# Kernel tuning notes

Measured on AMD Instinct MI355X. Metric: run time of the kernel, lower is better.

The kernel has to match this reference:

```python
import jax, jax.numpy as jnp
import numpy as np

D = 128      # embedding_dim
H = 8        # n_heads
L = 2        # n_encode_layers
FF = 512     # feed-forward hidden (4*D, AM default)
CLIP = 10.0  # tanh_clipping
EPS = 1e-5


def setup_inputs() -> dict:
    key = jax.random.key(0)
    ks = jax.random.split(key, 24)
    B, N = 32, 1000
    Nt = N + 2  # 2 depots + customers

    def w(k, shape, fan_in):
        return (jax.random.normal(k, shape, jnp.float32) / np.float32(np.sqrt(fan_in)))

    inp = {}
    inp["depot"] = jax.random.uniform(ks[0], (B, 2, 2), jnp.float32)
    inp["loc"] = jax.random.uniform(ks[1], (B, N, 2), jnp.float32)
    inp["demand"] = jax.random.uniform(ks[2], (B, N), jnp.float32)
    inp["mask"] = jax.random.randint(ks[3], (B, Nt), 0, 2) == 1
    # init embeddings
    inp["W_init_node"] = w(ks[4], (3, D), 3)
    inp["b_init_node"] = jnp.zeros((D,), jnp.float32)
    inp["W_init_depot"] = w(ks[5], (2, D), 2)
    inp["b_init_depot"] = jnp.zeros((D,), jnp.float32)
    # encoder layers (stacked over L)
    inp["enc_Wqkv"] = w(ks[6], (L, D, 3 * D), D)
    inp["enc_Wo"] = w(ks[7], (L, D, D), D)
    inp["enc_W1"] = w(ks[8], (L, D, FF), D)
    inp["enc_b1"] = jnp.zeros((L, FF), jnp.float32)
    inp["enc_W2"] = w(ks[9], (L, FF, D), FF)
    inp["enc_b2"] = jnp.zeros((L, D), jnp.float32)
    inp["bn1_s"] = jnp.ones((L, D), jnp.float32)
    inp["bn1_b"] = jnp.zeros((L, D), jnp.float32)
    inp["bn2_s"] = jnp.ones((L, D), jnp.float32)
    inp["bn2_b"] = jnp.zeros((L, D), jnp.float32)
    # decoder precompute / pointer attention
    inp["W_proj_node"] = w(ks[10], (D, 3 * D), D)   # project_node_embeddings_p2v
    inp["W_fixed_ctx"] = w(ks[11], (D, D), D)       # project_node_query_context
    inp["W_step_ctx"] = w(ks[12], (D, D), D)        # project_step_context_p2v
    inp["W_out"] = w(ks[13], (D, D), D)             # project_out_p2v
    return inp


def _bn(x, s, b):
    # BatchNorm1d over flattened (batch*nodes), training-mode stats, affine
    m = x.mean((0, 1))
    v = x.var((0, 1))
    return s * (x - m) * jax.lax.rsqrt(v + EPS) + b


def _mha(x, Wqkv, Wo):
    B, N, _ = x.shape
    dk = D // H
    q, k, v = jnp.split(x @ Wqkv, 3, axis=-1)

    def heads(t):
        return t.reshape(B, N, H, dk).transpose(0, 2, 1, 3)  # [B,H,N,dk]

    q, k, v = heads(q), heads(k), heads(v)
    attn = jax.nn.softmax(jnp.einsum('bhqd,bhkd->bhqk', q, k) / np.float32(np.sqrt(dk)), axis=-1)
    o = jnp.einsum('bhqk,bhkd->bhqd', attn, v).transpose(0, 2, 1, 3).reshape(B, N, D)
    return o @ Wo


def reference(depot, loc, demand, mask,
              W_init_node, b_init_node, W_init_depot, b_init_depot,
              enc_Wqkv, enc_Wo, enc_W1, enc_b1, enc_W2, enc_b2,
              bn1_s, bn1_b, bn2_s, bn2_b,
              W_proj_node, W_fixed_ctx, W_step_ctx, W_out):
    B = loc.shape[0]
    NEG = jnp.float32(-1e9)
    # --- init embeddings: depots via Linear(2,D), nodes via Linear(3,D) on (x,y,demand)
    depot_emb = depot @ W_init_depot + b_init_depot                      # [B,2,D]
    node_feat = jnp.concatenate([loc, demand[..., None]], -1)            # [B,N,3]
    node_emb = node_feat @ W_init_node + b_init_node                     # [B,N,D]
    h = jnp.concatenate([depot_emb, node_emb], 1)                        # [B,Nt,D]
    # --- graph encoder: L x (MHA + BN skip, FF + BN skip)
    for l in range(L):
        h = _bn(h + _mha(h, enc_Wqkv[l], enc_Wo[l]), bn1_s[l], bn1_b[l])
        ff = jax.nn.relu(h @ enc_W1[l] + enc_b1[l]) @ enc_W2[l] + enc_b2[l]
        h = _bn(h + ff, bn2_s[l], bn2_b[l])
    # --- fixed precompute (AttentionModelFixed)
    graph_embed = h.mean(1)                                              # [B,D]
    fixed_ctx = graph_embed @ W_fixed_ctx                                # [B,D]
    K_g, V_g, K_logit = jnp.split(h @ W_proj_node, 3, axis=-1)           # each [B,Nt,D]
    dk = D // H
    Kh = K_g.reshape(B, -1, H, dk).transpose(0, 2, 1, 3)                 # [B,H,Nt,dk]
    Vh = V_g.reshape(B, -1, H, dk).transpose(0, 2, 1, 3)
    # --- one glimpse+pointer step: context = fixed + projected first-depot step context
    query = fixed_ctx + h[:, 0, :] @ W_step_ctx                          # [B,D]
    qh = query.reshape(B, H, dk)                                         # [B,H,dk]
    compat = jnp.einsum('bhd,bhnd->bhn', qh, Kh) / np.float32(np.sqrt(dk))
    compat = jnp.where(mask[:, None, :], NEG, compat)                    # mask_inner
    attn = jax.nn.softmax(compat, axis=-1)
    glimpse = jnp.einsum('bhn,bhnd->bhd', attn, Vh).reshape(B, D) @ W_out
    logits = jnp.einsum('bd,bnd->bn', glimpse, K_logit) / np.float32(np.sqrt(D))
    logits = CLIP * jnp.tanh(logits)                                     # tanh clipping
    logits = jnp.where(mask, NEG, logits)                                # mask_logits
    log_p = jax.nn.log_softmax(logits, axis=-1)                          # [B,Nt]
    return log_p
```

## Files before the change

### kernel.cpp

```cpp
#include <hip/hip_runtime.h>

#define B_   32
#define NT_  1002
#define D_   128
#define H_   8
#define FF_  512
#define ROWS (B_ * NT_)
#define NEGV (-1e9f)
#define NTP  1024

typedef __bf16 bf16;
typedef __bf16 bf16x8 __attribute__((ext_vector_type(8)));
typedef __bf16 bf16x4 __attribute__((ext_vector_type(4)));
typedef float  f32x4  __attribute__((ext_vector_type(4)));
typedef float  f32x16 __attribute__((ext_vector_type(16)));

#if __has_builtin(__builtin_amdgcn_exp2f)
#define EXP2(x) __builtin_amdgcn_exp2f(x)
#else
#define EXP2(x) exp2f(x)
#endif

#define MFMA16(a, b, c) __builtin_amdgcn_mfma_f32_16x16x32_bf16(a, b, c, 0, 0, 0)

__device__ __forceinline__ int UNIT(int row, int seg) {
  return (row >> 4) * 64 + seg * 16 + (row & 15);
}
__device__ __forceinline__ int UNIT128(int row, int seg) {
  return (row >> 4) * 256 + seg * 16 + (row & 15);
}

#define SZ_QKV (2*384*128)
#define SZ_WO  (2*128*128)
#define SZ_W1  (2*512*128)
#define SZ_W2  (2*128*512)
#define SZ_PROJ (384*128)

__global__ __launch_bounds__(256) void prep_w(
    const float* __restrict__ qkv, const float* __restrict__ wo, const float* __restrict__ w1,
    const float* __restrict__ w2, const float* __restrict__ proj, bf16* __restrict__ out) {
  int i = blockIdx.x * 256 + threadIdx.x;
  int j = i;
  float v;
  if (j < SZ_QKV) {
    int l = j / 49152, r = j % 49152; int n = r >> 7, k = r & 127;
    v = qkv[((size_t)l * 128 + k) * 384 + n];
  } else {
    j -= SZ_QKV;
    if (j < SZ_WO) {
      int l = j >> 14, r = j & 16383; int n = r >> 7, k = r & 127;
      v = wo[((size_t)l * 128 + k) * 128 + n];
    } else {
      j -= SZ_WO;
      if (j < SZ_W1) {
        int l = j >> 16, r = j & 65535; int n = r >> 7, k = r & 127;
        v = w1[((size_t)l * 128 + k) * 512 + n];
      } else {
        j -= SZ_W1;
        if (j < SZ_W2) {
          int l = j >> 16, r = j & 65535; int n = r >> 9, k = r & 511;
          v = w2[((size_t)l * 512 + k) * 128 + n];
        } else {
          j -= SZ_W2;
          int n = j >> 7, k = j & 127;
          v = proj[(size_t)k * 384 + n];
        }
      }
    }
  }
  out[i] = (bf16)v;
}

__global__ __launch_bounds__(256) void init_kernel(
    const float* __restrict__ depot, const float* __restrict__ loc, const float* __restrict__ demand,
    const float* __restrict__ Wn, const float* __restrict__ bn_, const float* __restrict__ Wd,
    const float* __restrict__ bd, bf16* __restrict__ hb) {
  int idx = blockIdx.x * 256 + threadIdx.x;
  if (idx >= ROWS * D_) return;
  int c = idx & 127;
  int row = idx >> 7;
  int b = row / NT_;
  int n = row - b * NT_;
  float v;
  if (n < 2) {
    const float* dp = depot + (b * 2 + n) * 2;
    v = dp[0] * Wd[c] + dp[1] * Wd[D_ + c] + bd[c];
  } else {
    int i = n - 2;
    const float* lp = loc + ((size_t)b * 1000 + i) * 2;
    v = lp[0] * Wn[c] + lp[1] * Wn[D_ + c] + demand[b * 1000 + i] * Wn[2 * D_ + c] + bn_[c];
  }
  hb[idx] = (bf16)v;
}

template<int N_, int K_, bool BIAS, bool RELU, bool RES, bool STATS, bool BNA, bool BNR>
__global__ __launch_bounds__(256) void mgemm(
    const bf16* __restrict__ A, const bf16* __restrict__ Wt,
    const float* __restrict__ bias, const bf16* __restrict__ R, bf16* __restrict__ Cout,
    float* __restrict__ ps, float* __restrict__ pq,
    const float* __restrict__ miA, const float* __restrict__ miR) {
  __shared__ bf16 AsF[2048];
  __shared__ bf16 BsF[4096];
  __shared__ float sredS[4][64];
  __shared__ float sredQ[4][64];
  int tid = threadIdx.x;
  int w = tid >> 6, l = tid & 63;
  int bm = blockIdx.y * 64, bn = blockIdx.x * 128;
  int wr = (w >> 1) * 32, wc = (w & 1) * 64;
  f32x4 acc[2][4] = {};
  int srow = tid >> 2, sseg = tid & 3;
  int uA = UNIT(srow, sseg) * 8;
  int uB0 = UNIT(srow, sseg) * 8, uB1 = UNIT(srow + 64, sseg) * 8;
  for (int k0 = 0; k0 < K_; k0 += 32) {
    __syncthreads();
    {
      bf16x8 x = *(const bf16x8*)&A[(size_t)(bm + srow) * K_ + k0 + sseg * 8];
      if (BNA) {
        int kc = k0 + sseg * 8;
        f32x4 s0 = *(const f32x4*)&miA[kc],      s1 = *(const f32x4*)&miA[kc + 4];
        f32x4 c0 = *(const f32x4*)&miA[128 + kc], c1 = *(const f32x4*)&miA[128 + kc + 4];
        bf16x8 y;
#pragma unroll
        for (int i = 0; i < 4; ++i) y[i] = (bf16)__builtin_fmaf((float)x[i], s0[i], c0[i]);
#pragma unroll
        for (int i = 0; i < 4; ++i) y[4 + i] = (bf16)__builtin_fmaf((float)x[4 + i], s1[i], c1[i]);
        *(bf16x8*)&AsF[uA] = y;
      } else {
        *(bf16x8*)&AsF[uA] = x;
      }
    }
    *(bf16x8*)&BsF[uB0] = *(const bf16x8*)&Wt[(size_t)(bn + srow) * K_ + k0 + sseg * 8];
    *(bf16x8*)&BsF[uB1] = *(const bf16x8*)&Wt[(size_t)(bn + srow + 64) * K_ + k0 + sseg * 8];
    __syncthreads();
    bf16x8 af[2], bfr[4];
#pragma unroll
    for (int mi = 0; mi < 2; ++mi)
      af[mi] = *(const bf16x8*)&AsF[(((wr >> 4) + mi) * 64 + (l >> 4) * 16 + (l & 15)) * 8];
#pragma unroll
    for (int ni = 0; ni < 4; ++ni)
      bfr[ni] = *(const bf16x8*)&BsF[(((wc >> 4) + ni) * 64 + (l >> 4) * 16 + (l & 15)) * 8];
#pragma unroll
    for (int mi = 0; mi < 2; ++mi)
#pragma unroll
      for (int ni = 0; ni < 4; ++ni)
        acc[mi][ni] = MFMA16(af[mi], bfr[ni], acc[mi][ni]);
  }
  float scol[4] = {}, qcol[4] = {};
#pragma unroll
  for (int mi = 0; mi < 2; ++mi)
#pragma unroll
    for (int ni = 0; ni < 4; ++ni) {
      int col = bn + wc + ni * 16 + (l & 15);
      float rs = 1.f, rb = 0.f;
      if (RES && BNR) { rs = miR[col]; rb = miR[128 + col]; }
#pragma unroll
      for (int r = 0; r < 4; ++r) {
        int row = bm + wr + mi * 16 + (l >> 4) * 4 + r;
        float v = acc[mi][ni][r];
        if (BIAS) v += bias[col];
        if (RELU) v = fmaxf(v, 0.f);
        if (RES) {
          float x = (float)R[(size_t)row * N_ + col];
          v += BNR ? __builtin_fmaf(x, rs, rb) : x;
        }
        if (STATS) { scol[ni] += v; qcol[ni] += v * v; }
        Cout[(size_t)row * N_ + col] = (bf16)v;
      }
    }
  if (STATS) {
#pragma unroll
    for (int ni = 0; ni < 4; ++ni) {
      scol[ni] += __shfl_xor(scol[ni], 16); scol[ni] += __shfl_xor(scol[ni], 32);
      qcol[ni] += __shfl_xor(qcol[ni], 16); qcol[ni] += __shfl_xor(qcol[ni], 32);
    }
    __syncthreads();
    if (l < 16) {
#pragma unroll
      for (int ni = 0; ni < 4; ++ni) {
        sredS[w][ni * 16 + l] = scol[ni];
        sredQ[w][ni * 16 + l] = qcol[ni];
      }
    }
    __syncthreads();
    if (tid < 128) {
      int c = tid, cw = c >> 6, cc = c & 63;
      ps[(size_t)(bn + c) * 512 + blockIdx.y] = sredS[cw][cc] + sredS[cw + 2][cc];
      pq[(size_t)(bn + c) * 512 + blockIdx.y] = sredQ[cw][cc] + sredQ[cw + 2][cc];
    }
  }
}

template<bool BNA>
__global__ __launch_bounds__(256) void mgemm_qkv(
    const bf16* __restrict__ A, const bf16* __restrict__ Wt, const float* __restrict__ miA,
    bf16* __restrict__ Qh, bf16* __restrict__ Kh, bf16* __restrict__ Vh) {
  __shared__ bf16 smem[128 * 68];
  bf16* AsF = smem;
  bf16* BsF = smem + 2048;
  bf16* Vt2 = smem;
  int tid = threadIdx.x;
  int w = tid >> 6, l = tid & 63;
  int bm = blockIdx.y * 64, bn = blockIdx.x * 128;
  int wr = (w >> 1) * 32, wc = (w & 1) * 64;
  f32x4 acc[2][4] = {};
  int srow = tid >> 2, sseg = tid & 3;
  int uA = UNIT(srow, sseg) * 8;
  int uB0 = UNIT(srow, sseg) * 8, uB1 = UNIT(srow + 64, sseg) * 8;
  for (int k0 = 0; k0 < 128; k0 += 32) {
    __syncthreads();
    {
      bf16x8 x = *(const bf16x8*)&A[(size_t)(bm + srow) * 128 + k0 + sseg * 8];
      if (BNA) {
        int kc = k0 + sseg * 8;
        f32x4 s0 = *(const f32x4*)&miA[kc],      s1 = *(const f32x4*)&miA[kc + 4];
        f32x4 c0 = *(const f32x4*)&miA[128 + kc], c1 = *(const f32x4*)&miA[128 + kc + 4];
        bf16x8 y;
#pragma unroll
        for (int i = 0; i < 4; ++i) y[i] = (bf16)__builtin_fmaf((float)x[i], s0[i], c0[i]);
#pragma unroll
        for (int i = 0; i < 4; ++i) y[4 + i] = (bf16)__builtin_fmaf((float)x[4 + i], s1[i], c1[i]);
        *(bf16x8*)&AsF[uA] = y;
      } else {
        *(bf16x8*)&AsF[uA] = x;
      }
    }
    *(bf16x8*)&BsF[uB0] = *(const bf16x8*)&Wt[(size_t)(bn + srow) * 128 + k0 + sseg * 8];
    *(bf16x8*)&BsF[uB1] = *(const bf16x8*)&Wt[(size_t)(bn + srow + 64) * 128 + k0 + sseg * 8];
    __syncthreads();
    bf16x8 af[2], bfr[4];
#pragma unroll
    for (int mi = 0; mi < 2; ++mi)
      af[mi] = *(const bf16x8*)&AsF[(((wr >> 4) + mi) * 64 + (l >> 4) * 16 + (l & 15)) * 8];
#pragma unroll
    for (int ni = 0; ni < 4; ++ni)
      bfr[ni] = *(const bf16x8*)&BsF[(((wc >> 4) + ni) * 64 + (l >> 4) * 16 + (l & 15)) * 8];
#pragma unroll
    for (int mi = 0; mi < 2; ++mi)
#pragma unroll
      for (int ni = 0; ni < 4; ++ni)
        acc[mi][ni] = MFMA16(af[mi], bfr[ni], acc[mi][ni]);
  }
  if (blockIdx.x < 2) {
    bf16* dst = (blockIdx.x == 0) ? Qh : Kh;
#pragma unroll
    for (int ni = 0; ni < 4; ++ni) {
      int cl = wc + ni * 16 + (l & 15);
      int hd = cl >> 4, c16 = cl & 15;
#pragma unroll
      for (int mi = 0; mi < 2; ++mi)
#pragma unroll
        for (int r = 0; r < 4; ++r) {
          int row = bm + wr + mi * 16 + (l >> 4) * 4 + r;
          int b = row / NT_;
          int n = row - b * NT_;
          dst[(((size_t)b * 8 + hd) * NTP + n) * 16 + c16] = (bf16)acc[mi][ni][r];
        }
    }
  } else {
    __syncthreads();
#pragma unroll
    for (int mi = 0; mi < 2; ++mi)
#pragma unroll
      for (int ni = 0; ni < 4; ++ni) {
        int cl = wc + ni * 16 + (l & 15);
        int r0 = wr + mi * 16 + (l >> 4) * 4;
        bf16x4 pk;
#pragma unroll
        for (int r = 0; r < 4; ++r) pk[r] = (bf16)acc[mi][ni][r];
        *(bf16x4*)&Vt2[cl * 68 + r0] = pk;
      }
    __syncthreads();
    int colg = tid >> 4, nl = tid & 15;
#pragma unroll
    for (int ci = 0; ci < 8; ++ci) {
      int lc = colg + ci * 16;
      int hd = lc >> 4, c16 = lc & 15;
#pragma unroll
      for (int ri = 0; ri < 4; ++ri) {
        int lrow = nl + ri * 16;
        int row = bm + lrow;
        int b = row / NT_;
        int n = row - b * NT_;
        Vh[(((size_t)b * 8 + hd) * 16 + c16) * NTP + n] = Vt2[lc * 68 + lrow];
      }
    }
  }
}

__global__ __launch_bounds__(256) void fffused(
    const bf16* __restrict__ X, const float* __restrict__ mi,
    const bf16* __restrict__ W1t, const float* __restrict__ bias1,
    const bf16* __restrict__ W2t, const float* __restrict__ bias2,
    bf16* __restrict__ Y, float* __restrict__ ps, float* __restrict__ pq) {
  __shared__ bf16 A1[8192];
  __shared__ bf16 A2[8192];
  __shared__ bf16 BF[4096];
  __shared__ float sredS[4][64];
  __shared__ float sredQ[4][64];
  int tid = threadIdx.x;
  int w = tid >> 6, l = tid & 63;
  int bm = blockIdx.x * 64;
#pragma unroll
  for (int it = 0; it < 4; ++it) {
    int idx = it * 256 + tid;
    int row = idx >> 4, seg = idx & 15;
    bf16x8 x = *(const bf16x8*)&X[(size_t)(bm + row) * 128 + seg * 8];
    f32x4 s0 = *(const f32x4*)&mi[seg * 8],       s1 = *(const f32x4*)&mi[seg * 8 + 4];
    f32x4 c0 = *(const f32x4*)&mi[128 + seg * 8], c1 = *(const f32x4*)&mi[128 + seg * 8 + 4];
    bf16x8 y;
#pragma unroll
    for (int i = 0; i < 4; ++i) y[i] = (bf16)__builtin_fmaf((float)x[i], s0[i], c0[i]);
#pragma unroll
    for (int i = 0; i < 4; ++i) y[4 + i] = (bf16)__builtin_fmaf((float)x[4 + i], s1[i], c1[i]);
    *(bf16x8*)&A1[UNIT128(row, seg) * 8] = y;
  }
  int srow = tid >> 2, sseg = tid & 3;
  int uB0 = UNIT(srow, sseg) * 8, uB1 = UNIT(srow + 64, sseg) * 8;
  int wr = (w >> 1) * 32, wc = (w & 1) * 64;
  f32x4 acc2[2][4] = {};

  for (int nc = 0; nc < 4; ++nc) {
    f32x4 acc1[2][4] = {};
    for (int k0 = 0; k0 < 128; k0 += 32) {
      __syncthreads();
      *(bf16x8*)&BF[uB0] = *(const bf16x8*)&W1t[(size_t)(nc * 128 + srow) * 128 + k0 + sseg * 8];
      *(bf16x8*)&BF[uB1] = *(const bf16x8*)&W1t[(size_t)(nc * 128 + srow + 64) * 128 + k0 + sseg * 8];
      __syncthreads();
      bf16x8 af[2], hf[4];
#pragma unroll
      for (int m2 = 0; m2 < 2; ++m2)
        af[m2] = *(const bf16x8*)&BF[((w * 2 + m2) * 64 + (l >> 4) * 16 + (l & 15)) * 8];
#pragma unroll
      for (int ni = 0; ni < 4; ++ni)
        hf[ni] = *(const bf16x8*)&A1[(ni * 256 + ((k0 >> 3) + (l >> 4)) * 16 + (l & 15)) * 8];
#pragma unroll
      for (int m2 = 0; m2 < 2; ++m2)
#pragma unroll
        for (int ni = 0; ni < 4; ++ni)
          acc1[m2][ni] = MFMA16(af[m2], hf[ni], acc1[m2][ni]);
    }
#pragma unroll
    for (int m2 = 0; m2 < 2; ++m2) {
      int ffk0 = w * 32 + m2 * 16 + (l >> 4) * 4;
      int seg = ffk0 >> 3, half = ffk0 & 7;
#pragma unroll
      for (int ni = 0; ni < 4; ++ni) {
        bf16x4 pk;
#pragma unroll
        for (int r = 0; r < 4; ++r) {
          float v = acc1[m2][ni][r] + bias1[nc * 128 + ffk0 + r];
          pk[r] = (bf16)fmaxf(v, 0.f);
        }
        *(bf16x4*)&A2[(ni * 256 + seg * 16 + (l & 15)) * 8 + half] = pk;
      }
    }
    __syncthreads();
    for (int k0 = 0; k0 < 128; k0 += 32) {
      if (k0) __syncthreads();
      *(bf16x8*)&BF[uB0] = *(const bf16x8*)&W2t[(size_t)srow * 512 + nc * 128 + k0 + sseg * 8];
      *(bf16x8*)&BF[uB1] = *(const bf16x8*)&W2t[(size_t)(srow + 64) * 512 + nc * 128 + k0 + sseg * 8];
      __syncthreads();
      bf16x8 a2f[2], b2f[4];
#pragma unroll
      for (int m2 = 0; m2 < 2; ++m2)
        a2f[m2] = *(const bf16x8*)&A2[(((wr >> 4) + m2) * 256 + ((k0 >> 3) + (l >> 4)) * 16 + (l & 15)) * 8];
#pragma unroll
      for (int ni = 0; ni < 4; ++ni)
        b2f[ni] = *(const bf16x8*)&BF[(((wc >> 4) + ni) * 64 + (l >> 4) * 16 + (l & 15)) * 8];
#pragma unroll
      for (int m2 = 0; m2 < 2; ++m2)
#pragma unroll
        for (int ni = 0; ni < 4; ++ni)
          acc2[m2][ni] = MFMA16(a2f[m2], b2f[ni], acc2[m2][ni]);
    }
  }
  float scol[4] = {}, qcol[4] = {};
#pragma unroll
  for (int m2 = 0; m2 < 2; ++m2)
#pragma unroll
    for (int ni = 0; ni < 4; ++ni) {
      int col = wc + ni * 16 + (l & 15);
      float bb = bias2[col];
#pragma unroll
      for (int r = 0; r < 4; ++r) {
        int row = wr + m2 * 16 + (l >> 4) * 4 + r;
        float res = (float)A1[UNIT128(row, col >> 3) * 8 + (col & 7)];
        float v = acc2[m2][ni][r] + bb + res;
        scol[ni] += v; qcol[ni] += v * v;
        Y[(size_t)(bm + row) * 128 + col] = (bf16)v;
      }
    }
#pragma unroll
  for (int ni = 0; ni < 4; ++ni) {
    scol[ni] += __shfl_xor(scol[ni], 16); scol[ni] += __shfl_xor(scol[ni], 32);
    qcol[ni] += __shfl_xor(qcol[ni], 16); qcol[ni] += __shfl_xor(qcol[ni], 32);
  }
  __syncthreads();
  if (l < 16) {
#pragma unroll
    for (int ni = 0; ni < 4; ++ni) {
      sredS[w][ni * 16 + l] = scol[ni];
      sredQ[w][ni * 16 + l] = qcol[ni];
    }
  }
  __syncthreads();
  if (tid < 128) {
    int c = tid, cw = c >> 6, cc = c & 63;
    ps[(size_t)c * 512 + blockIdx.x] = sredS[cw][cc] + sredS[cw + 2][cc];
    pq[(size_t)c * 512 + blockIdx.x] = sredQ[cw][cc] + sredQ[cw + 2][cc];
  }
}

__global__ __launch_bounds__(256) void mattn(
    const bf16* __restrict__ Qh, const bf16* __restrict__ Kh,
    const bf16* __restrict__ Vh, bf16* __restrict__ ab) {
  __shared__ bf16 KsF[1024];
  __shared__ bf16 VtF[1024];
  __shared__ bf16 PsF[4][2048];
  int tid = threadIdx.x;
  int w = tid >> 6, l = tid & 63;
  int bh = blockIdx.x;
  int b = bh >> 3, hd = bh & 7;
  const bf16* Qp = Qh + (size_t)bh * NTP * 16;
  const bf16* Kp = Kh + (size_t)bh * NTP * 16;
  const bf16* Vp = Vh + (size_t)bh * 16 * NTP;
  int qbase = blockIdx.y * 128 + w * 32;
  int qrow = qbase + (l & 31); if (qrow >= NT_) qrow = NT_ - 1;
  bf16x8 qf = *(const bf16x8*)&Qp[qrow * 16 + (l >> 5) * 8];

  const float SC = 0.25f * 1.44269504088896f;
  const float MC = 8.0f * SC;
  f32x4 oacc[2] = {};
  f32x4 lacc[2] = {};
  bf16x8 ones;
#pragma unroll
  for (int i = 0; i < 8; ++i) ones[i] = (bf16)1.0f;
  const f32x16 zz = {0,0,0,0,0,0,0,0,0,0,0,0,0,0,0,0};

  for (int t = 0; t < 16; ++t) {
    int kb = t * 64;
    __syncthreads();
    if (tid < 128) {
      int key = (tid >> 6) * 32 + (tid & 31);
      int h2 = (tid >> 5) & 1;
      int krow = kb + key; if (krow >= NT_) krow = NT_ - 1;
      *(bf16x8*)&KsF[tid * 8] = *(const bf16x8*)&Kp[krow * 16 + h2 * 8];
    } else {
      int u = tid - 128;
      int seg = u >> 4, dim = u & 15;
      *(bf16x8*)&VtF[u * 8] = *(const bf16x8*)&Vp[dim * NTP + kb + seg * 8];
    }
    __syncthreads();

    f32x16 sv[2];
#pragma unroll
    for (int c = 0; c < 2; ++c) {
      bf16x8 kf = *(const bf16x8*)&KsF[(c * 64 + l) * 8];
      sv[c] = __builtin_amdgcn_mfma_f32_32x32x16_bf16(kf, qf, zz, 0, 0, 0);
    }
    if (kb + 64 > NT_) {
#pragma unroll
      for (int c = 0; c < 2; ++c)
#pragma unroll
        for (int r = 0; r < 16; ++r) {
          int key = kb + c * 32 + (r & 3) + 8 * (r >> 2) + 4 * (l >> 5);
          if (key >= NT_) sv[c][r] = -1e30f;
        }
    }
#pragma unroll
    for (int c = 0; c < 2; ++c)
#pragma unroll
      for (int r = 0; r < 16; ++r)
        sv[c][r] = EXP2(__builtin_fmaf(sv[c][r], SC, -MC));
    {
      int q = l & 31;
      int qh4 = q >> 4, ql = q & 15, half = (l >> 5) * 4;
#pragma unroll
      for (int c = 0; c < 2; ++c)
#pragma unroll
        for (int g2 = 0; g2 < 4; ++g2) {
          bf16x4 pk;
#pragma unroll
          for (int i = 0; i < 4; ++i) pk[i] = (bf16)sv[c][g2 * 4 + i];
          int unit = (c * 2 + qh4) * 64 + g2 * 16 + ql;
          *(bf16x4*)&PsF[w][unit * 8 + half] = pk;
        }
    }
#pragma unroll
    for (int kh = 0; kh < 2; ++kh) {
      bf16x8 vf = *(const bf16x8*)&VtF[(kh * 64 + l) * 8];
#pragma unroll
      for (int g = 0; g < 2; ++g) {
        bf16x8 pf = *(const bf16x8*)&PsF[w][((kh * 2 + g) * 64 + l) * 8];
        oacc[g] = MFMA16(pf, vf, oacc[g]);
        lacc[g] = MFMA16(pf, ones, lacc[g]);
      }
    }
  }
#pragma unroll
  for (int g = 0; g < 2; ++g)
#pragma unroll
    for (int r = 0; r < 4; ++r) {
      int qq = qbase + g * 16 + (l >> 4) * 4 + r;
      if (qq < NT_)
        ab[((size_t)b * NT_ + qq) * 128 + hd * 16 + (l & 15)] = (bf16)(oacc[g][r] / lacc[g][r]);
    }
}

__global__ __launch_bounds__(512) void stats_final(
    const float* __restrict__ ps, const float* __restrict__ pq,
    const float* __restrict__ sc, const float* __restrict__ bi, float* __restrict__ mi) {
  int tid = threadIdx.x;
  int c = tid >> 2, q4 = tid & 3;
  float s = 0.f, q = 0.f;
  for (int p = q4; p < 501; p += 4) { s += ps[c * 512 + p]; q += pq[c * 512 + p]; }
  s += __shfl_xor(s, 1); s += __shfl_xor(s, 2);
  q += __shfl_xor(q, 1); q += __shfl_xor(q, 2);
  if (q4 == 0) {
    float mean = s * (1.f / (float)ROWS);
    float var = q * (1.f / (float)ROWS) - mean * mean;
    float s2 = sc[c] * rsqrtf(var + 1e-5f);
    mi[c] = s2;
    mi[128 + c] = bi[c] - mean * s2;
  }
}

__global__ void ge_partial(const bf16* __restrict__ X, const float* __restrict__ mi,
                           float* __restrict__ part) {
  int b = blockIdx.x, ch = blockIdx.y, d = threadIdx.x;
  int n0 = ch * 126, n1 = n0 + 126; if (n1 > NT_) n1 = NT_;
  float sS = mi[d], sB = mi[128 + d];
  float s = 0.f;
  for (int n = n0; n < n1; ++n)
    s += __builtin_fmaf((float)X[((size_t)b * NT_ + n) * D_ + d], sS, sB);
  part[(b * 8 + ch) * D_ + d] = s;
}

__global__ void query_kernel(const float* __restrict__ part, const bf16* __restrict__ X,
                             const float* __restrict__ mi,
                             const float* __restrict__ Wf, const float* __restrict__ Ws,
                             float* __restrict__ qry) {
  __shared__ float sge[128], sh0[128];
  int b = blockIdx.x, d = threadIdx.x;
  float s = 0.f;
#pragma unroll
  for (int ch = 0; ch < 8; ++ch) s += part[(b * 8 + ch) * D_ + d];
  sge[d] = s * (1.f / (float)NT_);
  sh0[d] = __builtin_fmaf((float)X[(size_t)b * NT_ * D_ + d], mi[d], mi[128 + d]);
  __syncthreads();
  float q = 0.f;
  for (int k = 0; k < 128; ++k) q += sge[k] * Wf[k * D_ + d] + sh0[k] * Ws[k * D_ + d];
  qry[b * D_ + d] = q;
}

__global__ __launch_bounds__(256) void glimpse_kernel(
    const bf16* __restrict__ proj, const float* __restrict__ qry,
    const int* __restrict__ mask, float* __restrict__ glimpse) {
  int bid = blockIdx.x; int b = bid >> 3, hd = bid & 7;
  int tid = threadIdx.x;
  __shared__ float sq[16];
  __shared__ float sex[NT_];
  __shared__ float rmax[4];
  __shared__ float wacc[4][17];
  if (tid < 16) sq[tid] = qry[b * 128 + hd * 16 + tid];
  __syncthreads();
  const bf16* P = proj + (size_t)b * NT_ * 384;
  const int* Mk = mask + b * NT_;
  float lmax = -1e30f;
#pragma unroll
  for (int it = 0; it < 4; ++it) {
    int n = tid + it * 256;
    if (n < NT_) {
      float c = NEGV;
      if (!Mk[n]) {
        const bf16* kp = &P[(size_t)n * 384 + hd * 16];
        bf16x8 k0 = *(const bf16x8*)kp, k1 = *(const bf16x8*)(kp + 8);
        float d = 0.f;
#pragma unroll
        for (int i = 0; i < 8; ++i) d += sq[i] * (float)k0[i] + sq[8 + i] * (float)k1[i];
        c = d * 0.25f;
      }
      sex[n] = c;
      lmax = fmaxf(lmax, c);
    }
  }
#pragma unroll
  for (int o = 32; o > 0; o >>= 1) lmax = fmaxf(lmax, __shfl_xor(lmax, o));
  if ((tid & 63) == 0) rmax[tid >> 6] = lmax;
  __syncthreads();
  float mx = fmaxf(fmaxf(rmax[0], rmax[1]), fmaxf(rmax[2], rmax[3]));
  float acc[16];
#pragma unroll
  for (int i = 0; i < 16; ++i) acc[i] = 0.f;
  float lsum = 0.f;
#pragma unroll
  for (int it = 0; it < 4; ++it) {
    int n = tid + it * 256;
    if (n < NT_) {
      float e = __expf(sex[n] - mx);
      lsum += e;
      const bf16* vp = &P[(size_t)n * 384 + 128 + hd * 16];
      bf16x8 v0 = *(const bf16x8*)vp, v1 = *(const bf16x8*)(vp + 8);
#pragma unroll
      for (int i = 0; i < 8; ++i) { acc[i] += e * (float)v0[i]; acc[8 + i] += e * (float)v1[i]; }
    }
  }
#pragma unroll
  for (int o = 32; o > 0; o >>= 1) {
    lsum += __shfl_xor(lsum, o);
#pragma unroll
    for (int i = 0; i < 16; ++i) acc[i] += __shfl_xor(acc[i], o);
  }
  if ((tid & 63) == 0) {
    wacc[tid >> 6][16] = lsum;
#pragma unroll
    for (int i = 0; i < 16; ++i) wacc[tid >> 6][i] = acc[i];
  }
  __syncthreads();
  if (tid < 16) {
    float a = wacc[0][tid] + wacc[1][tid] + wacc[2][tid] + wacc[3][tid];
    float L = wacc[0][16] + wacc[1][16] + wacc[2][16] + wacc[3][16];
    glimpse[b * 128 + hd * 16 + tid] = a / L;
  }
}

__global__ void g2_kernel(const float* __restrict__ glimpse, const float* __restrict__ Wout,
                          float* __restrict__ g2) {
  __shared__ float sg[128];
  int b = blockIdx.x, d = threadIdx.x;
  sg[d] = glimpse[b * 128 + d];
  __syncthreads();
  float s = 0.f;
  for (int k = 0; k < 128; ++k) s += sg[k] * Wout[k * 128 + d];
  g2[b * 128 + d] = s;
}

__global__ __launch_bounds__(256) void logits_kernel(
    const bf16* __restrict__ proj, const float* __restrict__ g2,
    const int* __restrict__ mask, float* __restrict__ logits) {
  int b = blockIdx.y;
  int n = blockIdx.x * 256 + threadIdx.x;
  __shared__ float sg[128];
  if (threadIdx.x < 128) sg[threadIdx.x] = g2[b * 128 + threadIdx.x];
  __syncthreads();
  if (n >= NT_) return;
  const bf16* kp = &proj[((size_t)b * NT_ + n) * 384 + 256];
  float d = 0.f;
#pragma unroll
  for (int j = 0; j < 16; ++j) {
    bf16x8 v = *(const bf16x8*)&kp[j * 8];
#pragma unroll
    for (int i = 0; i < 8; ++i) d += sg[j * 8 + i] * (float)v[i];
  }
  d = 10.f * tanhf(d * 0.088388347648318447f);
  logits[b * NT_ + n] = mask[b * NT_ + n] ? NEGV : d;
}

__global__ __launch_bounds__(256) void lsm_kernel(const float* __restrict__ logits, float* __restrict__ out) {
  int b = blockIdx.x, tid = threadIdx.x;
  __shared__ float red[256];
  float mx = -1e30f;
  for (int n = tid; n < NT_; n += 256) mx = fmaxf(mx, logits[b * NT_ + n]);
  red[tid] = mx; __syncthreads();
  for (int s = 128; s > 0; s >>= 1) { if (tid < s) red[tid] = fmaxf(red[tid], red[tid + s]); __syncthreads(); }
  mx = red[0]; __syncthreads();
  float sm = 0.f;
  for (int n = tid; n < NT_; n += 256) sm += __expf(logits[b * NT_ + n] - mx);
  red[tid] = sm; __syncthreads();
  for (int s = 128; s > 0; s >>= 1) { if (tid < s) red[tid] += red[tid + s]; __syncthreads(); }
  float lse = mx + logf(red[0]);
  for (int n = tid; n < NT_; n += 256) out[(size_t)b * NT_ + n] = logits[b * NT_ + n] - lse;
}

extern "C" void kernel_launch(void* const* d_in, const int* in_sizes, int n_in,
                              void* d_out, int out_size, void* d_ws, size_t ws_size,
                              hipStream_t stream) {
  const float* depot        = (const float*)d_in[0];
  const float* loc          = (const float*)d_in[1];
  const float* demand       = (const float*)d_in[2];
  const int*   mask         = (const int*)d_in[3];
  const float* W_init_node  = (const float*)d_in[4];
  const float* b_init_node  = (const float*)d_in[5];
  const float* W_init_depot = (const float*)d_in[6];
  const float* b_init_depot = (const float*)d_in[7];
  const float* enc_Wqkv     = (const float*)d_in[8];
  const float* enc_Wo       = (const float*)d_in[9];
  const float* enc_W1       = (const float*)d_in[10];
  const float* enc_b1       = (const float*)d_in[11];
  const float* enc_W2       = (const float*)d_in[12];
  const float* enc_b2       = (const float*)d_in[13];
  const float* bn1_s        = (const float*)d_in[14];
  const float* bn1_b        = (const float*)d_in[15];
  const float* bn2_s        = (const float*)d_in[16];
  const float* bn2_b        = (const float*)d_in[17];
  const float* W_proj       = (const float*)d_in[18];
  const float* W_fixed      = (const float*)d_in[19];
  const float* W_step       = (const float*)d_in[20];
  const float* W_out        = (const float*)d_in[21];
  float* out = (float*)d_out;

  char* base = (char*)d_ws;
  bf16*  hb0   = (bf16*)(base);
  bf16*  ab    = (bf16*)(base + 8208384);
  bf16*  Qh    = (bf16*)(base + 16416768);
  bf16*  Kh    = (bf16*)(base + 24805376);
  bf16*  Vh    = (bf16*)(base + 33193984);
  bf16*  xb1   = Qh;
  bf16*  xb2   = (bf16*)(base + 41582592);
  bf16*  projb = (bf16*)(base + 49790976);
  bf16*  wb    = (bf16*)(base + 74416128);
  float* ps    = (float*)(base + 75300864);
  float* pq    = (float*)(base + 75563008);
  float* mi1   = (float*)(base + 75825152);
  float* mi2   = (float*)(base + 75826176);
  float* qry   = (float*)(base + 75827200);
  float* glim  = (float*)(base + 75843584);
  float* g2    = (float*)(base + 75859968);
  float* gep   = ps;
  float* logit = pq;

  bf16* wt_qkv  = wb;
  bf16* wt_wo   = wb + SZ_QKV;
  bf16* wt_w1   = wb + SZ_QKV + SZ_WO;
  bf16* wt_w2   = wb + SZ_QKV + SZ_WO + SZ_W1;
  bf16* wt_proj = wb + SZ_QKV + SZ_WO + SZ_W1 + SZ_W2;

  prep_w<<<1728, 256, 0, stream>>>(enc_Wqkv, enc_Wo, enc_W1, enc_W2, W_proj, wb);
  init_kernel<<<(ROWS * D_ + 255) / 256, 256, 0, stream>>>(
      depot, loc, demand, W_init_node, b_init_node, W_init_depot, b_init_depot, hb0);

  for (int l = 0; l < 2; ++l) {
    const bf16* hin = (l == 0) ? hb0 : xb2;
    if (l == 0)
      mgemm_qkv<false><<<dim3(3, 501), 256, 0, stream>>>(hin, wt_qkv, nullptr, Qh, Kh, Vh);
    else
      mgemm_qkv<true><<<dim3(3, 501), 256, 0, stream>>>(hin, wt_qkv + (size_t)384 * 128, mi2, Qh, Kh, Vh);
    mattn<<<dim3(256, 8), 256, 0, stream>>>(Qh, Kh, Vh, ab);
    if (l == 0)
      mgemm<128, 128, false, false, true, true, false, false><<<dim3(1, 501), 256, 0, stream>>>(
          ab, wt_wo, nullptr, hin, xb1, ps, pq, nullptr, nullptr);
    else
      mgemm<128, 128, false, false, true, true, false, true><<<dim3(1, 501), 256, 0, stream>>>(
          ab, wt_wo + (size_t)128 * 128, nullptr, hin, xb1, ps, pq, nullptr, mi2);
    stats_final<<<1, 512, 0, stream>>>(ps, pq, bn1_s + l * D_, bn1_b + l * D_, mi1);
    fffused<<<501, 256, 0, stream>>>(
        xb1, mi1, wt_w1 + (size_t)l * 512 * 128, enc_b1 + (size_t)l * FF_,
        wt_w2 + (size_t)l * 128 * 512, enc_b2 + (size_t)l * D_, xb2, ps, pq);
    stats_final<<<1, 512, 0, stream>>>(ps, pq, bn2_s + l * D_, bn2_b + l * D_, mi2);
  }

  mgemm<384, 128, false, false, false, false, true, false><<<dim3(3, 501), 256, 0, stream>>>(
      xb2, wt_proj, nullptr, nullptr, projb, nullptr, nullptr, mi2, nullptr);
  ge_partial<<<dim3(32, 8), 128, 0, stream>>>(xb2, mi2, gep);
  query_kernel<<<32, 128, 0, stream>>>(gep, xb2, mi2, W_fixed, W_step, qry);
  glimpse_kernel<<<256, 256, 0, stream>>>(projb, qry, mask, glim);
  g2_kernel<<<32, 128, 0, stream>>>(glim, W_out, g2);
  logits_kernel<<<dim3(4, 32), 256, 0, stream>>>(projb, g2, mask, logit);
  lsm_kernel<<<32, 256, 0, stream>>>(logit, out);
}
```

Measured before the change: 370.8 us.

## Stage full A tile once with XOR swizzle, read weights directly from global

The GEMM kernels (mgemm, mgemm_qkv, fffused) now load the whole 64x128 A tile into LDS once, using an XOR-swizzled layout meant to avoid bank conflicts. Weight fragments are read straight from global memory into MFMA operands instead of being staged through LDS. This removes the per-k-step LDS staging and barriers. The cost is uncoalesced, cache-dependent global loads for weights on every block, though the weights are small and should stay resident in L2.

New measurement: 400.8 us. 8.1% more time.

```diff
diff --git a/kernel.cpp b/kernel.cpp
--- a/kernel.cpp
+++ b/kernel.cpp
@@ -23,11 +23,8 @@
 
 #define MFMA16(a, b, c) __builtin_amdgcn_mfma_f32_16x16x32_bf16(a, b, c, 0, 0, 0)
 
-__device__ __forceinline__ int UNIT(int row, int seg) {
-  return (row >> 4) * 64 + seg * 16 + (row & 15);
-}
-__device__ __forceinline__ int UNIT128(int row, int seg) {
-  return (row >> 4) * 256 + seg * 16 + (row & 15);
+__device__ __forceinline__ int UNITX(int row, int seg) {
+  return (row >> 4) * 256 + seg * 16 + ((row & 15) ^ seg);
 }
 
 #define SZ_QKV (2*384*128)
@@ -93,52 +90,57 @@
   hb[idx] = (bf16)v;
 }
 
-template<int N_, int K_, bool BIAS, bool RELU, bool RES, bool STATS, bool BNA, bool BNR>
+template<bool BNA>
+__device__ __forceinline__ void stageA(
+    bf16* __restrict__ A1, const bf16* __restrict__ A, int bm, int tid,
+    const float* __restrict__ miA) {
+#pragma unroll
+  for (int it = 0; it < 4; ++it) {
+    int idx = it * 256 + tid;
+    int row = idx >> 4, seg = idx & 15;
+    bf16x8 x = *(const bf16x8*)&A[(size_t)(bm + row) * 128 + seg * 8];
+    if (BNA) {
+      int kc = seg * 8;
+      f32x4 s0 = *(const f32x4*)&miA[kc],       s1 = *(const f32x4*)&miA[kc + 4];
+      f32x4 c0 = *(const f32x4*)&miA[128 + kc], c1 = *(const f32x4*)&miA[128 + kc + 4];
+      bf16x8 y;
+#pragma unroll
+      for (int i = 0; i < 4; ++i) y[i] = (bf16)__builtin_fmaf((float)x[i], s0[i], c0[i]);
+#pragma unroll
+      for (int i = 0; i < 4; ++i) y[4 + i] = (bf16)__builtin_fmaf((float)x[4 + i], s1[i], c1[i]);
+      *(bf16x8*)&A1[UNITX(row, seg) * 8] = y;
+    } else {
+      *(bf16x8*)&A1[UNITX(row, seg) * 8] = x;
+    }
+  }
+}
+
+template<int N_, bool BIAS, bool RELU, bool RES, bool STATS, bool BNA, bool BNR>
 __global__ __launch_bounds__(256) void mgemm(
     const bf16* __restrict__ A, const bf16* __restrict__ Wt,
     const float* __restrict__ bias, const bf16* __restrict__ R, bf16* __restrict__ Cout,
     float* __restrict__ ps, float* __restrict__ pq,
     const float* __restrict__ miA, const float* __restrict__ miR) {
-  __shared__ bf16 AsF[2048];
-  __shared__ bf16 BsF[4096];
+  __shared__ bf16 A1[8192];
   __shared__ float sredS[4][64];
   __shared__ float sredQ[4][64];
   int tid = threadIdx.x;
   int w = tid >> 6, l = tid & 63;
   int bm = blockIdx.y * 64, bn = blockIdx.x * 128;
   int wr = (w >> 1) * 32, wc = (w & 1) * 64;
+  stageA<BNA>(A1, A, bm, tid, miA);
+  __syncthreads();
   f32x4 acc[2][4] = {};
-  int srow = tid >> 2, sseg = tid & 3;
-  int uA = UNIT(srow, sseg) * 8;
-  int uB0 = UNIT(srow, sseg) * 8, uB1 = UNIT(srow + 64, sseg) * 8;
-  for (int k0 = 0; k0 < K_; k0 += 32) {
-    __syncthreads();
-    {
-      bf16x8 x = *(const bf16x8*)&A[(size_t)(bm + srow) * K_ + k0 + sseg * 8];
-      if (BNA) {
-        int kc = k0 + sseg * 8;
-        f32x4 s0 = *(const f32x4*)&miA[kc],      s1 = *(const f32x4*)&miA[kc + 4];
-        f32x4 c0 = *(const f32x4*)&miA[128 + kc], c1 = *(const f32x4*)&miA[128 + kc + 4];
-        bf16x8 y;
-#pragma unroll
-        for (int i = 0; i < 4; ++i) y[i] = (bf16)__builtin_fmaf((float)x[i], s0[i], c0[i]);
-#pragma unroll
-        for (int i = 0; i < 4; ++i) y[4 + i] = (bf16)__builtin_fmaf((float)x[4 + i], s1[i], c1[i]);
-        *(bf16x8*)&AsF[uA] = y;
-      } else {
-        *(bf16x8*)&AsF[uA] = x;
-      }
-    }
-    *(bf16x8*)&BsF[uB0] = *(const bf16x8*)&Wt[(size_t)(bn + srow) * K_ + k0 + sseg * 8];
-    *(bf16x8*)&BsF[uB1] = *(const bf16x8*)&Wt[(size_t)(bn + srow + 64) * K_ + k0 + sseg * 8];
-    __syncthreads();
+#pragma unroll
+  for (int k0 = 0; k0 < 4; ++k0) {
+    int seg = k0 * 4 + (l >> 4);
     bf16x8 af[2], bfr[4];
 #pragma unroll
     for (int mi = 0; mi < 2; ++mi)
-      af[mi] = *(const bf16x8*)&AsF[(((wr >> 4) + mi) * 64 + (l >> 4) * 16 + (l & 15)) * 8];
+      af[mi] = *(const bf16x8*)&A1[((((wr >> 4) + mi) * 16 + seg) * 16 + ((l & 15) ^ seg)) * 8];
 #pragma unroll
     for (int ni = 0; ni < 4; ++ni)
-      bfr[ni] = *(const bf16x8*)&BsF[(((wc >> 4) + ni) * 64 + (l >> 4) * 16 + (l & 15)) * 8];
+      bfr[ni] = *(const bf16x8*)&Wt[(size_t)(bn + wc + ni * 16 + (l & 15)) * 128 + k0 * 32 + (l >> 4) * 8];
 #pragma unroll
     for (int mi = 0; mi < 2; ++mi)
 #pragma unroll
@@ -194,46 +196,26 @@
 __global__ __launch_bounds__(256) void mgemm_qkv(
     const bf16* __restrict__ A, const bf16* __restrict__ Wt, const float* __restrict__ miA,
     bf16* __restrict__ Qh, bf16* __restrict__ Kh, bf16* __restrict__ Vh) {
-  __shared__ bf16 smem[128 * 68];
-  bf16* AsF = smem;
-  bf16* BsF = smem + 2048;
+  __shared__ bf16 smem[8704];
+  bf16* A1 = smem;
   bf16* Vt2 = smem;
   int tid = threadIdx.x;
   int w = tid >> 6, l = tid & 63;
   int bm = blockIdx.y * 64, bn = blockIdx.x * 128;
   int wr = (w >> 1) * 32, wc = (w & 1) * 64;
+  stageA<BNA>(A1, A, bm, tid, miA);
+  __syncthreads();
   f32x4 acc[2][4] = {};
-  int srow = tid >> 2, sseg = tid & 3;
-  int uA = UNIT(srow, sseg) * 8;
-  int uB0 = UNIT(srow, sseg) * 8, uB1 = UNIT(srow + 64, sseg) * 8;
-  for (int k0 = 0; k0 < 128; k0 += 32) {
-    __syncthreads();
-    {
-      bf16x8 x = *(const bf16x8*)&A[(size_t)(bm + srow) * 128 + k0 + sseg * 8];
-      if (BNA) {
-        int kc = k0 + sseg * 8;
-        f32x4 s0 = *(const f32x4*)&miA[kc],      s1 = *(const f32x4*)&miA[kc + 4];
-        f32x4 c0 = *(const f32x4*)&miA[128 + kc], c1 = *(const f32x4*)&miA[128 + kc + 4];
-        bf16x8 y;
-#pragma unroll
-        for (int i = 0; i < 4; ++i) y[i] = (bf16)__builtin_fmaf((float)x[i], s0[i], c0[i]);
-#pragma unroll
-        for (int i = 0; i < 4; ++i) y[4 + i] = (bf16)__builtin_fmaf((float)x[4 + i], s1[i], c1[i]);
-        *(bf16x8*)&AsF[uA] = y;
-      } else {
-        *(bf16x8*)&AsF[uA] = x;
-      }
-    }
-    *(bf16x8*)&BsF[uB0] = *(const bf16x8*)&Wt[(size_t)(bn + srow) * 128 + k0 + sseg * 8];
-    *(bf16x8*)&BsF[uB1] = *(const bf16x8*)&Wt[(size_t)(bn + srow + 64) * 128 + k0 + sseg * 8];
-    __syncthreads();
+#pragma unroll
+  for (int k0 = 0; k0 < 4; ++k0) {
+    int seg = k0 * 4 + (l >> 4);
     bf16x8 af[2], bfr[4];
 #pragma unroll
     for (int mi = 0; mi < 2; ++mi)
-      af[mi] = *(const bf16x8*)&AsF[(((wr >> 4) + mi) * 64 + (l >> 4) * 16 + (l & 15)) * 8];
+      af[mi] = *(const bf16x8*)&A1[((((wr >> 4) + mi) * 16 + seg) * 16 + ((l & 15) ^ seg)) * 8];
 #pragma unroll
     for (int ni = 0; ni < 4; ++ni)
-      bfr[ni] = *(const bf16x8*)&BsF[(((wc >> 4) + ni) * 64 + (l >> 4) * 16 + (l & 15)) * 8];
+      bfr[ni] = *(const bf16x8*)&Wt[(size_t)(bn + wc + ni * 16 + (l & 15)) * 128 + k0 * 32 + (l >> 4) * 8];
 #pragma unroll
     for (int mi = 0; mi < 2; ++mi)
 #pragma unroll
@@ -294,51 +276,35 @@
     bf16* __restrict__ Y, float* __restrict__ ps, float* __restrict__ pq) {
   __shared__ bf16 A1[8192];
   __shared__ bf16 A2[8192];
-  __shared__ bf16 BF[4096];
   __shared__ float sredS[4][64];
   __shared__ float sredQ[4][64];
   int tid = threadIdx.x;
   int w = tid >> 6, l = tid & 63;
   int bm = blockIdx.x * 64;
-#pragma unroll
-  for (int it = 0; it < 4; ++it) {
-    int idx = it * 256 + tid;
-    int row = idx >> 4, seg = idx & 15;
-    bf16x8 x = *(const bf16x8*)&X[(size_t)(bm + row) * 128 + seg * 8];
-    f32x4 s0 = *(const f32x4*)&mi[seg * 8],       s1 = *(const f32x4*)&mi[seg * 8 + 4];
-    f32x4 c0 = *(const f32x4*)&mi[128 + seg * 8], c1 = *(const f32x4*)&mi[128 + seg * 8 + 4];
-    bf16x8 y;
-#pragma unroll
-    for (int i = 0; i < 4; ++i) y[i] = (bf16)__builtin_fmaf((float)x[i], s0[i], c0[i]);
-#pragma unroll
-    for (int i = 0; i < 4; ++i) y[4 + i] = (bf16)__builtin_fmaf((float)x[4 + i], s1[i], c1[i]);
-    *(bf16x8*)&A1[UNIT128(row, seg) * 8] = y;
-  }
-  int srow = tid >> 2, sseg = tid & 3;
-  int uB0 = UNIT(srow, sseg) * 8, uB1 = UNIT(srow + 64, sseg) * 8;
+  stageA<true>(A1, X, bm, tid, mi);
+  __syncthreads();
   int wr = (w >> 1) * 32, wc = (w & 1) * 64;
   f32x4 acc2[2][4] = {};
 
   for (int nc = 0; nc < 4; ++nc) {
     f32x4 acc1[2][4] = {};
-    for (int k0 = 0; k0 < 128; k0 += 32) {
-      __syncthreads();
-      *(bf16x8*)&BF[uB0] = *(const bf16x8*)&W1t[(size_t)(nc * 128 + srow) * 128 + k0 + sseg * 8];
-      *(bf16x8*)&BF[uB1] = *(const bf16x8*)&W1t[(size_t)(nc * 128 + srow + 64) * 128 + k0 + sseg * 8];
-      __syncthreads();
+#pragma unroll
+    for (int k0 = 0; k0 < 4; ++k0) {
+      int seg = k0 * 4 + (l >> 4);
       bf16x8 af[2], hf[4];
 #pragma unroll
       for (int m2 = 0; m2 < 2; ++m2)
-        af[m2] = *(const bf16x8*)&BF[((w * 2 + m2) * 64 + (l >> 4) * 16 + (l & 15)) * 8];
+        af[m2] = *(const bf16x8*)&W1t[(size_t)(nc * 128 + w * 32 + m2 * 16 + (l & 15)) * 128 + k0 * 32 + (l >> 4) * 8];
 #pragma unroll
       for (int ni = 0; ni < 4; ++ni)
-        hf[ni] = *(const bf16x8*)&A1[(ni * 256 + ((k0 >> 3) + (l >> 4)) * 16 + (l & 15)) * 8];
+        hf[ni] = *(const bf16x8*)&A1[((ni * 16 + seg) * 16 + ((l & 15) ^ seg)) * 8];
 #pragma unroll
       for (int m2 = 0; m2 < 2; ++m2)
 #pragma unroll
         for (int ni = 0; ni < 4; ++ni)
           acc1[m2][ni] = MFMA16(af[m2], hf[ni], acc1[m2][ni]);
     }
+    __syncthreads();
 #pragma unroll
     for (int m2 = 0; m2 < 2; ++m2) {
       int ffk0 = w * 32 + m2 * 16 + (l >> 4) * 4;
@@ -355,18 +321,15 @@
       }
     }
     __syncthreads();
-    for (int k0 = 0; k0 < 128; k0 += 32) {
-      if (k0) __syncthreads();
-      *(bf16x8*)&BF[uB0] = *(const bf16x8*)&W2t[(size_t)srow * 512 + nc * 128 + k0 + sseg * 8];
-      *(bf16x8*)&BF[uB1] = *(const bf16x8*)&W2t[(size_t)(srow + 64) * 512 + nc * 128 + k0 + sseg * 8];
-      __syncthreads();
+#pragma unroll
+    for (int k0 = 0; k0 < 4; ++k0) {
       bf16x8 a2f[2], b2f[4];
 #pragma unroll
       for (int m2 = 0; m2 < 2; ++m2)
-        a2f[m2] = *(const bf16x8*)&A2[(((wr >> 4) + m2) * 256 + ((k0 >> 3) + (l >> 4)) * 16 + (l & 15)) * 8];
+        a2f[m2] = *(const bf16x8*)&A2[(((wr >> 4) + m2) * 256 + (k0 * 4 + (l >> 4)) * 16 + (l & 15)) * 8];
 #pragma unroll
       for (int ni = 0; ni < 4; ++ni)
-        b2f[ni] = *(const bf16x8*)&BF[(((wc >> 4) + ni) * 64 + (l >> 4) * 16 + (l & 15)) * 8];
+        b2f[ni] = *(const bf16x8*)&W2t[(size_t)(wc + ni * 16 + (l & 15)) * 512 + nc * 128 + k0 * 32 + (l >> 4) * 8];
 #pragma unroll
       for (int m2 = 0; m2 < 2; ++m2)
 #pragma unroll
@@ -384,7 +347,7 @@
 #pragma unroll
       for (int r = 0; r < 4; ++r) {
         int row = wr + m2 * 16 + (l >> 4) * 4 + r;
-        float res = (float)A1[UNIT128(row, col >> 3) * 8 + (col & 7)];
+        float res = (float)A1[UNITX(row, col >> 3) * 8 + (col & 7)];
         float v = acc2[m2][ni][r] + bb + res;
         scol[ni] += v; qcol[ni] += v * v;
         Y[(size_t)(bm + row) * 128 + col] = (bf16)v;
@@ -737,10 +700,10 @@
       mgemm_qkv<true><<<dim3(3, 501), 256, 0, stream>>>(hin, wt_qkv + (size_t)384 * 128, mi2, Qh, Kh, Vh);
     mattn<<<dim3(256, 8), 256, 0, stream>>>(Qh, Kh, Vh, ab);
     if (l == 0)
-      mgemm<128, 128, false, false, true, true, false, false><<<dim3(1, 501), 256, 0, stream>>>(
+      mgemm<128, false, false, true, true, false, false><<<dim3(1, 501), 256, 0, stream>>>(
           ab, wt_wo, nullptr, hin, xb1, ps, pq, nullptr, nullptr);
     else
-      mgemm<128, 128, false, false, true, true, false, true><<<dim3(1, 501), 256, 0, stream>>>(
+      mgemm<128, false, false, true, true, false, true><<<dim3(1, 501), 256, 0, stream>>>(
           ab, wt_wo + (size_t)128 * 128, nullptr, hin, xb1, ps, pq, nullptr, mi2);
     stats_final<<<1, 512, 0, stream>>>(ps, pq, bn1_s + l * D_, bn1_b + l * D_, mi1);
     fffused<<<501, 256, 0, stream>>>(
@@ -749,7 +712,7 @@
     stats_final<<<1, 512, 0, stream>>>(ps, pq, bn2_s + l * D_, bn2_b + l * D_, mi2);
   }
 
-  mgemm<384, 128, false, false, false, false, true, false><<<dim3(3, 501), 256, 0, stream>>>(
+  mgemm<384, false, false, false, false, true, false><<<dim3(3, 501), 256, 0, stream>>>(
       xb2, wt_proj, nullptr, nullptr, projb, nullptr, nullptr, mi2, nullptr);
   ge_partial<<<dim3(32, 8), 128, 0, stream>>>(xb2, mi2, gep);
   query_kernel<<<32, 128, 0, stream>>>(gep, xb2, mi2, W_fixed, W_step, qry);
```

## Keep attention probabilities in registers via permlane32 swap instead of LDS

Applied to the files above, without the earlier changes.

The encoder attention kernel no longer writes the exponentiated scores to shared memory and reads them back for the PV product. Scores from the 32x32 MFMA are packed to bf16 and rearranged across lane halves with permlane32_swap, which turns them directly into the A operand of a second 32x32 MFMA. A column of ones in the B operand computes the softmax denominator in the same MFMA, replacing the separate row-sum MFMAs. This removes the per-tile LDS round trip and frees shared memory. In exchange, half of the PV MFMA output columns hold padding zeros, and normalisation now needs a shuffle at the end.

Measured after the change: 387.7 us. 1.05x slower.

```diff
diff --git a/kernel.cpp b/kernel.cpp
--- a/kernel.cpp
+++ b/kernel.cpp
@@ -22,6 +22,13 @@
 #endif
 
 #define MFMA16(a, b, c) __builtin_amdgcn_mfma_f32_16x16x32_bf16(a, b, c, 0, 0, 0)
+#define MFMA32(a, b, c) __builtin_amdgcn_mfma_f32_32x32x16_bf16(a, b, c, 0, 0, 0)
+
+__device__ __forceinline__ unsigned pkbf(float lo, float hi) {
+  unsigned r;
+  asm("v_cvt_pk_bf16_f32 %0, %1, %2" : "=v"(r) : "v"(lo), "v"(hi));
+  return r;
+}
 
 __device__ __forceinline__ int UNIT(int row, int seg) {
   return (row >> 4) * 64 + seg * 16 + (row & 15);
@@ -117,7 +124,7 @@
       bf16x8 x = *(const bf16x8*)&A[(size_t)(bm + srow) * K_ + k0 + sseg * 8];
       if (BNA) {
         int kc = k0 + sseg * 8;
-        f32x4 s0 = *(const f32x4*)&miA[kc],      s1 = *(const f32x4*)&miA[kc + 4];
+        f32x4 s0 = *(const f32x4*)&miA[kc],       s1 = *(const f32x4*)&miA[kc + 4];
         f32x4 c0 = *(const f32x4*)&miA[128 + kc], c1 = *(const f32x4*)&miA[128 + kc + 4];
         bf16x8 y;
 #pragma unroll
@@ -212,7 +219,7 @@
       bf16x8 x = *(const bf16x8*)&A[(size_t)(bm + srow) * 128 + k0 + sseg * 8];
       if (BNA) {
         int kc = k0 + sseg * 8;
-        f32x4 s0 = *(const f32x4*)&miA[kc],      s1 = *(const f32x4*)&miA[kc + 4];
+        f32x4 s0 = *(const f32x4*)&miA[kc],       s1 = *(const f32x4*)&miA[kc + 4];
         f32x4 c0 = *(const f32x4*)&miA[128 + kc], c1 = *(const f32x4*)&miA[128 + kc + 4];
         bf16x8 y;
 #pragma unroll
@@ -416,7 +423,6 @@
     const bf16* __restrict__ Vh, bf16* __restrict__ ab) {
   __shared__ bf16 KsF[1024];
   __shared__ bf16 VtF[1024];
-  __shared__ bf16 PsF[4][2048];
   int tid = threadIdx.x;
   int w = tid >> 6, l = tid & 63;
   int bh = blockIdx.x;
@@ -430,12 +436,12 @@
 
   const float SC = 0.25f * 1.44269504088896f;
   const float MC = 8.0f * SC;
-  f32x4 oacc[2] = {};
-  f32x4 lacc[2] = {};
-  bf16x8 ones;
-#pragma unroll
-  for (int i = 0; i < 8; ++i) ones[i] = (bf16)1.0f;
   const f32x16 zz = {0,0,0,0,0,0,0,0,0,0,0,0,0,0,0,0};
+  f32x16 oacc = zz;
+  bf16x8 ones8, zero8;
+#pragma unroll
+  for (int i = 0; i < 8; ++i) { ones8[i] = (bf16)1.0f; zero8[i] = (bf16)0.0f; }
+  int d31 = l & 31;
 
   for (int t = 0; t < 16; ++t) {
     int kb = t * 64;
@@ -452,59 +458,48 @@
     }
     __syncthreads();
 
-    f32x16 sv[2];
 #pragma unroll
     for (int c = 0; c < 2; ++c) {
       bf16x8 kf = *(const bf16x8*)&KsF[(c * 64 + l) * 8];
-      sv[c] = __builtin_amdgcn_mfma_f32_32x32x16_bf16(kf, qf, zz, 0, 0, 0);
-    }
-    if (kb + 64 > NT_) {
-#pragma unroll
-      for (int c = 0; c < 2; ++c)
+      f32x16 sv = MFMA32(kf, qf, zz);
+      if (kb + 64 > NT_) {
 #pragma unroll
         for (int r = 0; r < 16; ++r) {
           int key = kb + c * 32 + (r & 3) + 8 * (r >> 2) + 4 * (l >> 5);
-          if (key >= NT_) sv[c][r] = -1e30f;
+          if (key >= NT_) sv[r] = -1e30f;
         }
-    }
-#pragma unroll
-    for (int c = 0; c < 2; ++c)
+      }
 #pragma unroll
       for (int r = 0; r < 16; ++r)
-        sv[c][r] = EXP2(__builtin_fmaf(sv[c][r], SC, -MC));
-    {
-      int q = l & 31;
-      int qh4 = q >> 4, ql = q & 15, half = (l >> 5) * 4;
-#pragma unroll
-      for (int c = 0; c < 2; ++c)
-#pragma unroll
-        for (int g2 = 0; g2 < 4; ++g2) {
-          bf16x4 pk;
-#pragma unroll
-          for (int i = 0; i < 4; ++i) pk[i] = (bf16)sv[c][g2 * 4 + i];
-          int unit = (c * 2 + qh4) * 64 + g2 * 16 + ql;
-          *(bf16x4*)&PsF[w][unit * 8 + half] = pk;
-        }
-    }
-#pragma unroll
-    for (int kh = 0; kh < 2; ++kh) {
-      bf16x8 vf = *(const bf16x8*)&VtF[(kh * 64 + l) * 8];
-#pragma unroll
-      for (int g = 0; g < 2; ++g) {
-        bf16x8 pf = *(const bf16x8*)&PsF[w][((kh * 2 + g) * 64 + l) * 8];
-        oacc[g] = MFMA16(pf, vf, oacc[g]);
-        lacc[g] = MFMA16(pf, ones, lacc[g]);
-      }
-    }
-  }
-#pragma unroll
-  for (int g = 0; g < 2; ++g)
-#pragma unroll
-    for (int r = 0; r < 4; ++r) {
-      int qq = qbase + g * 16 + (l >> 4) * 4 + r;
-      if (qq < NT_)
-        ab[((size_t)b * NT_ + qq) * 128 + hd * 16 + (l & 15)] = (bf16)(oacc[g][r] / lacc[g][r]);
-    }
+        sv[r] = EXP2(__builtin_fmaf(sv[r], SC, -MC));
+#pragma unroll
+      for (int kk2 = 0; kk2 < 2; ++kk2) {
+        int o = kk2 * 8;
+        unsigned a0 = pkbf(sv[o + 0], sv[o + 1]);
+        unsigned a1 = pkbf(sv[o + 2], sv[o + 3]);
+        unsigned b0 = pkbf(sv[o + 4], sv[o + 5]);
+        unsigned b1 = pkbf(sv[o + 6], sv[o + 7]);
+        auto s01 = __builtin_amdgcn_permlane32_swap(a0, b0, false, false);
+        auto s23 = __builtin_amdgcn_permlane32_swap(a1, b1, false, false);
+        union { unsigned u[4]; bf16x8 v; } pu;
+        pu.u[0] = s01[0]; pu.u[1] = s23[0]; pu.u[2] = s01[1]; pu.u[3] = s23[1];
+        int kkG = c * 2 + kk2;
+        bf16x8 vb;
+        if (d31 < 16)       vb = *(const bf16x8*)&VtF[((kkG * 2 + (l >> 5)) * 16 + d31) * 8];
+        else if (d31 == 16) vb = ones8;
+        else                vb = zero8;
+        oacc = MFMA32(pu.v, vb, oacc);
+      }
+    }
+  }
+#pragma unroll
+  for (int r = 0; r < 16; ++r) {
+    float ls = __shfl(oacc[r], (l & 32) + 16);
+    int qw = (r & 3) + 8 * (r >> 2) + 4 * (l >> 5);
+    int qq = qbase + qw;
+    if (d31 < 16 && qq < NT_)
+      ab[((size_t)b * NT_ + qq) * 128 + hd * 16 + d31] = (bf16)(oacc[r] / ls);
+  }
 }
 
 __global__ __launch_bounds__(512) void stats_final(
```
